# Kernel tuning notes

Hardware: AMD Instinct MI355X
Metric: run time of the kernel (lower is better)

## Reference

```python
import jax, jax.numpy as jnp
import numpy as np

E = 4        # num_edge_types
C = 4        # num_channels (must equal E due to module's layer>0 einsum)
N = 2048     # num_nodes
W_IN = 256
W_OUT = 128


def _xavier_uniform(key, shape):
    # torch.nn.init.xavier_uniform_ on a 2D tensor [fan_out, fan_in] style
    fan_out, fan_in = shape[0], shape[1]
    bound = float(np.sqrt(6.0 / (fan_in + fan_out)))
    return jax.random.uniform(key, shape, jnp.float32, -bound, bound)


def setup_inputs() -> dict:
    key = jax.random.key(0)
    k = jax.random.split(key, 7)
    A = jax.random.uniform(k[0], (E, N, N), jnp.float32)   # non-negative dense multi-relation adjacency
    X = jax.random.normal(k[1], (N, W_IN), jnp.float32)
    gt_w1 = _xavier_uniform(k[2], (C, E))   # layer0 conv1
    gt_w2 = _xavier_uniform(k[3], (C, E))   # layer0 conv2
    gt_w3 = _xavier_uniform(k[4], (C, C))   # layer1 conv1 (C == E)
    gcn_w = _xavier_uniform(k[5], (W_IN, W_OUT))
    gcn_b = jnp.zeros((W_OUT,), jnp.float32)
    return {"A": A, "X": X, "gt_w1": gt_w1, "gt_w2": gt_w2, "gt_w3": gt_w3,
            "gcn_w": gcn_w, "gcn_b": gcn_b}


def _normalize_adj(adj):
    # adj: [N, N]. Symmetric degree normalization D^-1/2 (A+I) D^-1/2,
    # expressed as broadcasted row/col scaling (math-identical to the
    # original diag-matmul-matmul formulation).
    adj = adj + jnp.eye(adj.shape[0], dtype=adj.dtype)
    deg = adj.sum(axis=1)
    d = deg ** -0.5
    d = jnp.where(jnp.isinf(d), jnp.zeros_like(d), d)
    return d[:, None] * adj * d[None, :]


def reference(A, X, gt_w1, gt_w2, gt_w3, gcn_w, gcn_b):
    # --- GT layer 0 (first=True): two softmax-weighted mixes of A, then bmm ---
    fw1 = jax.nn.softmax(gt_w1, axis=1)
    fw2 = jax.nn.softmax(gt_w2, axis=1)
    Ha = jnp.einsum('oi,inm->onm', fw1, A)   # [C, N, N]
    Hb = jnp.einsum('oi,inm->onm', fw2, A)   # [C, N, N]
    H = jnp.matmul(Ha, Hb)                   # [C, N, N]
    # --- GT layer 1 (first=False): H @ (softmax mix of A) ---
    fw3 = jax.nn.softmax(gt_w3, axis=1)
    Hc = jnp.einsum('oi,inm->onm', fw3, A)   # [C, N, N]
    H = jnp.matmul(H, Hc)                    # [C, N, N]
    # --- per-channel degree-normalized GCN conv ---
    Hn = jax.vmap(_normalize_adj)(H)         # [C, N, N]
    support = X @ gcn_w                      # [N, W_OUT] (shared across channels)
    out = jnp.einsum('cnm,mf->cnf', Hn, support) + gcn_b  # [C, N, W_OUT]
    out = jax.nn.relu(out)
    # torch.cat(X_out, dim=1): channel blocks side by side -> [N, C*W_OUT]
    return jnp.transpose(out, (1, 0, 2)).reshape(N, C * W_OUT)
```

## Files before the change

kernel.cpp:

```cpp
#include <hip/hip_runtime.h>
#include <math.h>

#define N_NODES 2048
#define NNE ((long)N_NODES * N_NODES)

#define SUPD_SCALE 8192.0f

typedef _Float16 half4_t __attribute__((ext_vector_type(4)));
typedef _Float16 half8_t __attribute__((ext_vector_type(8)));
typedef float    floatx4 __attribute__((ext_vector_type(4)));

__device__ __forceinline__ void async_cp16(const void* g, void* l) {
  __builtin_amdgcn_global_load_lds((const __attribute__((address_space(1))) void*)g,
                                   (__attribute__((address_space(3))) void*)l,
                                   16, 0, 0);
}

__device__ __forceinline__ float colscale_from(float cn) {
  return exp2f((float)(10 - ilogbf(fmaxf(cn, 1e-37f))));
}

__global__ void softmax3_zero_k(const float* __restrict__ w1,
                                const float* __restrict__ w2,
                                const float* __restrict__ w3,
                                float* __restrict__ fw,
                                float* __restrict__ cn) {
  int t = threadIdx.x;
  float4 z4 = {0.f, 0.f, 0.f, 0.f};
  ((float4*)cn)[t] = z4;
  if (t < 12) {
    const float* src = (t < 4) ? w1 : (t < 8) ? w2 : w3;
    int r = t & 3;
    float v0 = src[r * 4 + 0], v1 = src[r * 4 + 1];
    float v2 = src[r * 4 + 2], v3 = src[r * 4 + 3];
    float m = fmaxf(fmaxf(v0, v1), fmaxf(v2, v3));
    float e0 = expf(v0 - m), e1 = expf(v1 - m), e2 = expf(v2 - m), e3 = expf(v3 - m);
    float inv = 1.0f / (e0 + e1 + e2 + e3);
    fw[t * 4 + 0] = e0 * inv; fw[t * 4 + 1] = e1 * inv;
    fw[t * 4 + 2] = e2 * inv; fw[t * 4 + 3] = e3 * inv;
  }
}

__global__ __launch_bounds__(128)
void support_k(const float* __restrict__ X, const float* __restrict__ W,
               float* __restrict__ sup) {
  __shared__ float Xs[256];
  const int t = threadIdx.x;
  const int m = blockIdx.x;
  Xs[t]       = X[(long)m * 256 + t];
  Xs[t + 128] = X[(long)m * 256 + t + 128];
  __syncthreads();
  float acc = 0.f;
  #pragma unroll 8
  for (int k = 0; k < 256; ++k) acc = fmaf(Xs[k], W[(long)k * 128 + t], acc);
  sup[(long)m * 128 + t] = acc;
}

__global__ __launch_bounds__(256)
void rc_from_A_k(const float* __restrict__ A, const float* __restrict__ fw,
                 float* __restrict__ rc) {
  __shared__ float red[4][4];
  const int r = blockIdx.x;
  const int w = threadIdx.x >> 6, lane = threadIdx.x & 63;
  float se[4];
  #pragma unroll
  for (int e = 0; e < 4; ++e) {
    const float4* row = (const float4*)(A + (long)e * NNE + (long)r * N_NODES);
    float s = 0.f;
    #pragma unroll
    for (int q = 0; q < 2; ++q) {
      float4 a = row[w * 128 + q * 64 + lane];
      s += (a.x + a.y) + (a.z + a.w);
    }
    se[e] = s;
  }
  float m[4];
  #pragma unroll
  for (int c = 0; c < 4; ++c)
    m[c] = fw[32 + c * 4 + 0] * se[0] + fw[32 + c * 4 + 1] * se[1] +
           fw[32 + c * 4 + 2] * se[2] + fw[32 + c * 4 + 3] * se[3];
  #pragma unroll
  for (int o = 32; o > 0; o >>= 1) {
    #pragma unroll
    for (int c = 0; c < 4; ++c) m[c] += __shfl_down(m[c], o, 64);
  }
  if (lane == 0) {
    #pragma unroll
    for (int c = 0; c < 4; ++c) red[w][c] = m[c];
  }
  __syncthreads();
  if (threadIdx.x < 4) {
    int c = threadIdx.x;
    rc[c * N_NODES + r] = (red[0][c] + red[1][c]) + (red[2][c] + red[3][c]);
  }
}

__global__ __launch_bounds__(256)
void matvecA_k(const float* __restrict__ A, const float* __restrict__ fw, int off,
               const float* __restrict__ vin, float* __restrict__ vout) {
  __shared__ float red[4][4];
  const int r = blockIdx.x;
  const int w = threadIdx.x >> 6, lane = threadIdx.x & 63;
  float acc[4][4] = {{0.f}};
  #pragma unroll
  for (int q = 0; q < 2; ++q) {
    const int j4 = w * 128 + q * 64 + lane;
    float4 v0 = *(const float4*)&vin[0 * 2048 + j4 * 4];
    float4 v1 = *(const float4*)&vin[1 * 2048 + j4 * 4];
    float4 v2 = *(const float4*)&vin[2 * 2048 + j4 * 4];
    float4 v3 = *(const float4*)&vin[3 * 2048 + j4 * 4];
    #pragma unroll
    for (int e = 0; e < 4; ++e) {
      float4 a = *(const float4*)(A + (long)e * NNE + (long)r * N_NODES + j4 * 4);
      acc[e][0] += (a.x * v0.x + a.y * v0.y) + (a.z * v0.z + a.w * v0.w);
      acc[e][1] += (a.x * v1.x + a.y * v1.y) + (a.z * v1.z + a.w * v1.w);
      acc[e][2] += (a.x * v2.x + a.y * v2.y) + (a.z * v2.z + a.w * v2.w);
      acc[e][3] += (a.x * v3.x + a.y * v3.y) + (a.z * v3.z + a.w * v3.w);
    }
  }
  float m[4];
  #pragma unroll
  for (int c = 0; c < 4; ++c)
    m[c] = fw[off + c * 4 + 0] * acc[0][c] + fw[off + c * 4 + 1] * acc[1][c] +
           fw[off + c * 4 + 2] * acc[2][c] + fw[off + c * 4 + 3] * acc[3][c];
  #pragma unroll
  for (int o = 32; o > 0; o >>= 1) {
    #pragma unroll
    for (int c = 0; c < 4; ++c) m[c] += __shfl_down(m[c], o, 64);
  }
  if (lane == 0) {
    #pragma unroll
    for (int c = 0; c < 4; ++c) red[w][c] = m[c];
  }
  __syncthreads();
  if (threadIdx.x < 4) {
    int c = threadIdx.x;
    vout[c * N_NODES + r] = (red[0][c] + red[1][c]) + (red[2][c] + red[3][c]);
  }
}

__global__ __launch_bounds__(256)
void transposeV_k(const float* __restrict__ sup, const float* __restrict__ deg,
                  float* __restrict__ dvec, float* __restrict__ supd,
                  _Float16* __restrict__ TH, _Float16* __restrict__ TL,
                  float* __restrict__ cn0) {
  __shared__ _Float16 sh[32][33], sl[32][33];
  __shared__ float red[8][32];
  const int t = threadIdx.x;
  const int z = blockIdx.z;
  const int m0 = blockIdx.x * 32, f0 = blockIdx.y * 32;
  const int r0 = t >> 5, col = t & 31;
  float part = 0.f;
  #pragma unroll
  for (int m = 0; m < 4; ++m) {
    const int row = m0 + r0 + 8 * m;
    float dm = 1.0f / sqrtf(1.0f + deg[(long)z * N_NODES + row]);
    float sv = sup[(long)row * 128 + f0 + col] * dm;
    supd[((long)z * N_NODES + row) * 128 + f0 + col] = sv;
    if (blockIdx.y == 0 && col == 0) dvec[(long)z * N_NODES + row] = dm;
    float v = sv * SUPD_SCALE;
    _Float16 h = (_Float16)v;
    sh[r0 + 8 * m][col] = h;
    sl[r0 + 8 * m][col] = (_Float16)(v - (float)h);
    part += fabsf(v);
  }
  red[r0][col] = part;
  __syncthreads();
  if (t < 32) {
    float s = 0.f;
    #pragma unroll
    for (int q = 0; q < 8; ++q) s += red[q][t];
    atomicAdd(&cn0[(long)z * 128 + f0 + t], s);
  }
  const int rr = t >> 3, cq = (t & 7) * 4;
  half4_t oh, ol;
  #pragma unroll
  for (int d = 0; d < 4; ++d) { oh[d] = sh[cq + d][rr]; ol[d] = sl[cq + d][rr]; }
  long ob = (long)z * 128 * N_NODES + (long)(f0 + rr) * N_NODES + m0 + cq;
  *(half4_t*)(TH + ob) = oh;
  *(half4_t*)(TL + ob) = ol;
}

__global__ __launch_bounds__(256, 4)
void gemm_mix_k(const float* __restrict__ A, const float* __restrict__ fw, int off,
                const _Float16* __restrict__ BH, const _Float16* __restrict__ BL,
                float* __restrict__ C) {
  __shared__ __align__(16) _Float16 Hs[2][2][1024];
  __shared__ __align__(16) _Float16 Bs[2][2][4096];

  const int t = threadIdx.x;
  const int lane = t & 63;
  const int w = t >> 6;
  const int bid = blockIdx.x;
  const int tile = bid & 63;
  const int ch = (bid >> 6) & 3;
  const int kc = bid >> 8;
  const int i0 = tile * 32;
  const long koff = (long)kc * 512;

  float wv[4];
  #pragma unroll
  for (int e = 0; e < 4; ++e) wv[e] = fw[off + ch * 4 + e];

  const int rr = t >> 3;
  const int k4 = (t & 7) * 4;
  const float* gA = A + (long)(i0 + rr) * N_NODES + koff + k4;
  const int hoff = rr * 32 + (((k4 >> 3) + (rr >> 1)) & 3) * 8 + (k4 & 7);

  const int hls = w >> 1;
  const int half = w & 1;
  const int kc_st = (((lane & 3) - ((lane >> 3) & 3)) & 3) * 8;
  const _Float16* gB = (hls ? BL : BH)
                     + ((long)ch * 128 + half * 64 + (lane >> 2)) * (long)N_NODES
                     + koff + kc_st;

  const int wm = w >> 1, wn = w & 1;
  const int fr = lane & 15;
  const int fq = lane >> 4;
  const int fkz = ((fq + (fr >> 1)) & 3) * 8;
  const int aoff = (wm * 16 + fr) * 32 + fkz;

  floatx4 acc[4];
  #pragma unroll
  for (int j = 0; j < 4; ++j) {
    floatx4 zz4 = {0.f, 0.f, 0.f, 0.f};
    acc[j] = zz4;
  }

  const int NKT = 16;

  auto stageB = [&](int ktv, int pb) {
    _Float16* lb = &Bs[pb][hls][half * 2048];
    const _Float16* g = gB + ktv * 32;
    #pragma unroll
    for (int q = 0; q < 4; ++q)
      async_cp16(g + (long)q * (16L * N_NODES), lb + q * 512 + lane * 8);
  };
  auto mixStore = [&](const float4& a0, const float4& a1,
                      const float4& a2, const float4& a3, int pb) {
    float av0[4] = {a0.x, a0.y, a0.z, a0.w};
    float av1[4] = {a1.x, a1.y, a1.z, a1.w};
    float av2[4] = {a2.x, a2.y, a2.z, a2.w};
    float av3[4] = {a3.x, a3.y, a3.z, a3.w};
    half4_t h, l;
    #pragma unroll
    for (int d = 0; d < 4; ++d) {
      float o = wv[0] * av0[d] + wv[1] * av1[d] + wv[2] * av2[d] + wv[3] * av3[d];
      _Float16 hh = (_Float16)o;
      h[d] = hh; l[d] = (_Float16)(o - (float)hh);
    }
    *(half4_t*)&Hs[pb][0][hoff] = h;
    *(half4_t*)&Hs[pb][1][hoff] = l;
  };

  {
    float4 a0 = *(const float4*)(gA);
    float4 a1 = *(const float4*)(gA + NNE);
    float4 a2 = *(const float4*)(gA + 2 * NNE);
    float4 a3 = *(const float4*)(gA + 3 * NNE);
    stageB(0, 0);
    mixStore(a0, a1, a2, a3, 0);
  }
  __syncthreads();

  for (int kt = 0; kt < NKT; ++kt) {
    const int p = kt & 1;
    float4 a0, a1, a2, a3;
    if (kt + 1 < NKT) {
      const float* g = gA + (kt + 1) * 32;
      a0 = *(const float4*)(g);
      a1 = *(const float4*)(g + NNE);
      a2 = *(const float4*)(g + 2 * NNE);
      a3 = *(const float4*)(g + 3 * NNE);
      stageB(kt + 1, p ^ 1);
    }
    half8_t ah = *(const half8_t*)&Hs[p][0][aoff];
    half8_t al = *(const half8_t*)&Hs[p][1][aoff];
    #pragma unroll
    for (int nt = 0; nt < 4; ++nt) {
      const int bo = (wn * 64 + nt * 16 + fr) * 32 + fkz;
      half8_t bh = *(const half8_t*)&Bs[p][0][bo];
      half8_t bl = *(const half8_t*)&Bs[p][1][bo];
      acc[nt] = __builtin_amdgcn_mfma_f32_16x16x32_f16(ah, bh, acc[nt], 0, 0, 0);
      acc[nt] = __builtin_amdgcn_mfma_f32_16x16x32_f16(al, bh, acc[nt], 0, 0, 0);
      acc[nt] = __builtin_amdgcn_mfma_f32_16x16x32_f16(ah, bl, acc[nt], 0, 0, 0);
    }
    if (kt + 1 < NKT) mixStore(a0, a1, a2, a3, p ^ 1);
    __syncthreads();
  }

  const int er = fq * 4;
  const int ec = lane & 15;
  float* Cb = C + ((long)(kc * 4 + ch) * N_NODES + i0 + wm * 16) * 128;
  #pragma unroll
  for (int nt = 0; nt < 4; ++nt) {
    const int f = wn * 64 + nt * 16 + ec;
    #pragma unroll
    for (int r = 0; r < 4; ++r)
      Cb[(long)(er + r) * 128 + f] = acc[nt][r];
  }
}

__global__ __launch_bounds__(256)
void combineT_k(const float* __restrict__ P, int parts,
                const float* __restrict__ cn_in, float* __restrict__ cn_out,
                _Float16* __restrict__ TH, _Float16* __restrict__ TL) {
  __shared__ _Float16 sh[32][33], sl[32][33];
  __shared__ float red[8][32];
  const int t = threadIdx.x;
  const int z = blockIdx.z;
  const int j0 = blockIdx.x * 32, f0 = blockIdx.y * 32;
  const int r0 = t >> 5, col = t & 31;
  const float s = colscale_from(cn_in[(long)z * 128 + f0 + col]);
  const long step = 4L * N_NODES * 128;
  float part = 0.f;
  #pragma unroll
  for (int m = 0; m < 4; ++m) {
    long idx = ((long)z * N_NODES + j0 + r0 + 8 * m) * 128 + f0 + col;
    float v = (P[idx] + P[idx + step]) + (P[idx + 2 * step] + P[idx + 3 * step]);
    v *= s;
    _Float16 h = (_Float16)v;
    sh[r0 + 8 * m][col] = h;
    sl[r0 + 8 * m][col] = (_Float16)(v - (float)h);
    part += fabsf(v);
  }
  if (cn_out) red[r0][col] = part;
  __syncthreads();
  if (cn_out && t < 32) {
    float ss = 0.f;
    #pragma unroll
    for (int q = 0; q < 8; ++q) ss += red[q][t];
    atomicAdd(&cn_out[(long)z * 128 + f0 + t], ss);
  }
  const int rr = t >> 3, cq = (t & 7) * 4;
  half4_t oh, ol;
  #pragma unroll
  for (int d = 0; d < 4; ++d) { oh[d] = sh[cq + d][rr]; ol[d] = sl[cq + d][rr]; }
  long ob = (long)z * 128 * N_NODES + (long)(f0 + rr) * N_NODES + j0 + cq;
  *(half4_t*)(TH + ob) = oh;
  *(half4_t*)(TL + ob) = ol;
}

__global__ __launch_bounds__(256)
void final_k(const float4* __restrict__ T2, const float4* __restrict__ supd,
             const float* __restrict__ dvec, const float* __restrict__ cn0,
             const float* __restrict__ cn1, const float* __restrict__ bias,
             float* __restrict__ out) {
  const int t = threadIdx.x;
  const int z = blockIdx.y;
  const int idx = blockIdx.x * 256 + t;
  const int i = idx >> 5;
  const int fq = (idx & 31) * 4;
  const long step4 = 4L * N_NODES * 32;
  long b4 = (long)z * N_NODES * 32 + idx;
  float4 s0 = T2[b4];
  float4 s1 = T2[b4 + step4];
  float4 s2 = T2[b4 + 2 * step4];
  float4 s3 = T2[b4 + 3 * step4];
  float4 sp = supd[(long)z * N_NODES * 32 + idx];
  const float dn = dvec[(long)z * N_NODES + i];
  float inv[4];
  #pragma unroll
  for (int d = 0; d < 4; ++d) {
    int i0 = ilogbf(fmaxf(cn0[(long)z * 128 + fq + d], 1e-37f));
    int i1 = ilogbf(fmaxf(cn1[(long)z * 128 + fq + d], 1e-37f));
    inv[d] = exp2f((float)(i0 + i1 - 33));
  }
  float4 o;
  o.x = fmaxf(dn * (((s0.x + s1.x) + (s2.x + s3.x)) * inv[0] + sp.x) + bias[fq + 0], 0.f);
  o.y = fmaxf(dn * (((s0.y + s1.y) + (s2.y + s3.y)) * inv[1] + sp.y) + bias[fq + 1], 0.f);
  o.z = fmaxf(dn * (((s0.z + s1.z) + (s2.z + s3.z)) * inv[2] + sp.z) + bias[fq + 2], 0.f);
  o.w = fmaxf(dn * (((s0.w + s1.w) + (s2.w + s3.w)) * inv[3] + sp.w) + bias[fq + 3], 0.f);
  *(float4*)(out + (long)i * 512 + z * 128 + fq) = o;
}

extern "C" void kernel_launch(void* const* d_in, const int* in_sizes, int n_in,
                              void* d_out, int out_size, void* d_ws, size_t ws_size,
                              hipStream_t stream) {
  const float* A  = (const float*)d_in[0];
  const float* X  = (const float*)d_in[1];
  const float* w1 = (const float*)d_in[2];
  const float* w2 = (const float*)d_in[3];
  const float* w3 = (const float*)d_in[4];
  const float* gw = (const float*)d_in[5];
  const float* gb = (const float*)d_in[6];
  float* out = (float*)d_out;

  float* ws   = (float*)d_ws;
  float* fw   = ws;
  float* rc   = fw + 64;
  float* v1   = rc + 4 * N_NODES;
  float* deg  = v1 + 4 * N_NODES;
  float* dvec = deg + 4 * N_NODES;
  float* sup  = dvec + 4 * N_NODES;
  float* cn0  = sup + (long)N_NODES * 128;
  float* cn1  = cn0 + 512;
  float* supd = cn1 + 512;
  float* Mtmp = supd + 4L * N_NODES * 128;
  _Float16* arena = (_Float16*)(Mtmp + 16L * N_NODES * 128);
  _Float16* VTH = arena;
  _Float16* VTL = VTH + 4L * 128 * N_NODES;
  _Float16* T0H = VTL + 4L * 128 * N_NODES;
  _Float16* T0L = T0H + 4L * 128 * N_NODES;
  _Float16* T1H = T0L + 4L * 128 * N_NODES;
  _Float16* T1L = T1H + 4L * 128 * N_NODES;

  softmax3_zero_k<<<1, 256, 0, stream>>>(w1, w2, w3, fw, cn0);
  support_k<<<N_NODES, 128, 0, stream>>>(X, gw, sup);
  rc_from_A_k<<<N_NODES, 256, 0, stream>>>(A, fw, rc);
  matvecA_k<<<N_NODES, 256, 0, stream>>>(A, fw, 16, rc, v1);
  matvecA_k<<<N_NODES, 256, 0, stream>>>(A, fw, 0, v1, deg);
  transposeV_k<<<dim3(64, 4, 4), 256, 0, stream>>>(sup, deg, dvec, supd,
                                                   VTH, VTL, cn0);
  gemm_mix_k<<<1024, 256, 0, stream>>>(A, fw, 32, VTH, VTL, Mtmp);
  combineT_k<<<dim3(64, 4, 4), 256, 0, stream>>>(Mtmp, 4, cn0, cn1, T0H, T0L);
  gemm_mix_k<<<1024, 256, 0, stream>>>(A, fw, 16, T0H, T0L, Mtmp);
  combineT_k<<<dim3(64, 4, 4), 256, 0, stream>>>(Mtmp, 4, cn1, nullptr, T1H, T1L);
  gemm_mix_k<<<1024, 256, 0, stream>>>(A, fw, 0, T1H, T1L, Mtmp);
  final_k<<<dim3(256, 4), 256, 0, stream>>>((const float4*)Mtmp,
                                            (const float4*)supd, dvec,
                                            cn0, cn1, gb, out);
}
```

Baseline: 259.7 us.

## Load GEMM B operands directly into registers and drop the supd buffer

The GEMM kernel stops staging the B tiles (high/low fp16 halves) through LDS with async global-to-LDS copies. Each wave now loads its MFMA B fragments straight from global memory into registers, double-buffered across two k-steps, and the LDS B buffer and the occupancy hint in the launch bounds are removed. Separately, the intermediate supd buffer is no longer written; final_k rebuilds that term from sup scaled by dn squared. The aims are lower LDS traffic and footprint and one fewer global write and read, at the cost of more VGPRs and less coalesced, possibly redundant global loads of B across waves.

```diff
diff --git a/kernel.cpp b/kernel.cpp
--- a/kernel.cpp
+++ b/kernel.cpp
@@ -9,12 +9,6 @@
 typedef _Float16 half4_t __attribute__((ext_vector_type(4)));
 typedef _Float16 half8_t __attribute__((ext_vector_type(8)));
 typedef float    floatx4 __attribute__((ext_vector_type(4)));
-
-__device__ __forceinline__ void async_cp16(const void* g, void* l) {
-  __builtin_amdgcn_global_load_lds((const __attribute__((address_space(1))) void*)g,
-                                   (__attribute__((address_space(3))) void*)l,
-                                   16, 0, 0);
-}
 
 __device__ __forceinline__ float colscale_from(float cn) {
   return exp2f((float)(10 - ilogbf(fmaxf(cn, 1e-37f))));
@@ -141,7 +135,7 @@
 
 __global__ __launch_bounds__(256)
 void transposeV_k(const float* __restrict__ sup, const float* __restrict__ deg,
-                  float* __restrict__ dvec, float* __restrict__ supd,
+                  float* __restrict__ dvec,
                   _Float16* __restrict__ TH, _Float16* __restrict__ TL,
                   float* __restrict__ cn0) {
   __shared__ _Float16 sh[32][33], sl[32][33];
@@ -156,7 +150,6 @@
     const int row = m0 + r0 + 8 * m;
     float dm = 1.0f / sqrtf(1.0f + deg[(long)z * N_NODES + row]);
     float sv = sup[(long)row * 128 + f0 + col] * dm;
-    supd[((long)z * N_NODES + row) * 128 + f0 + col] = sv;
     if (blockIdx.y == 0 && col == 0) dvec[(long)z * N_NODES + row] = dm;
     float v = sv * SUPD_SCALE;
     _Float16 h = (_Float16)v;
@@ -181,12 +174,11 @@
   *(half4_t*)(TL + ob) = ol;
 }
 
-__global__ __launch_bounds__(256, 4)
+__global__ __launch_bounds__(256)
 void gemm_mix_k(const float* __restrict__ A, const float* __restrict__ fw, int off,
                 const _Float16* __restrict__ BH, const _Float16* __restrict__ BL,
                 float* __restrict__ C) {
   __shared__ __align__(16) _Float16 Hs[2][2][1024];
-  __shared__ __align__(16) _Float16 Bs[2][2][4096];
 
   const int t = threadIdx.x;
   const int lane = t & 63;
@@ -207,19 +199,16 @@
   const float* gA = A + (long)(i0 + rr) * N_NODES + koff + k4;
   const int hoff = rr * 32 + (((k4 >> 3) + (rr >> 1)) & 3) * 8 + (k4 & 7);
 
-  const int hls = w >> 1;
-  const int half = w & 1;
-  const int kc_st = (((lane & 3) - ((lane >> 3) & 3)) & 3) * 8;
-  const _Float16* gB = (hls ? BL : BH)
-                     + ((long)ch * 128 + half * 64 + (lane >> 2)) * (long)N_NODES
-                     + koff + kc_st;
-
   const int wm = w >> 1, wn = w & 1;
   const int fr = lane & 15;
   const int fq = lane >> 4;
   const int fkz = ((fq + (fr >> 1)) & 3) * 8;
   const int aoff = (wm * 16 + fr) * 32 + fkz;
 
+  const long bbase = ((long)(ch * 128 + wn * 64 + fr)) * N_NODES + koff + fq * 8;
+  const _Float16* gBH = BH + bbase;
+  const _Float16* gBL = BL + bbase;
+
   floatx4 acc[4];
   #pragma unroll
   for (int j = 0; j < 4; ++j) {
@@ -227,65 +216,64 @@
     acc[j] = zz4;
   }
 
-  const int NKT = 16;
-
-  auto stageB = [&](int ktv, int pb) {
-    _Float16* lb = &Bs[pb][hls][half * 2048];
-    const _Float16* g = gB + ktv * 32;
-    #pragma unroll
-    for (int q = 0; q < 4; ++q)
-      async_cp16(g + (long)q * (16L * N_NODES), lb + q * 512 + lane * 8);
+  float4 aA[4], aB[4];
+  half8_t b0h[4], b0l[4], b1h[4], b1l[4];
+
+  auto loadA = [&](float4* av, int kt) {
+    const float* g = gA + kt * 32;
+    av[0] = *(const float4*)(g);
+    av[1] = *(const float4*)(g + NNE);
+    av[2] = *(const float4*)(g + 2 * NNE);
+    av[3] = *(const float4*)(g + 3 * NNE);
   };
-  auto mixStore = [&](const float4& a0, const float4& a1,
-                      const float4& a2, const float4& a3, int pb) {
-    float av0[4] = {a0.x, a0.y, a0.z, a0.w};
-    float av1[4] = {a1.x, a1.y, a1.z, a1.w};
-    float av2[4] = {a2.x, a2.y, a2.z, a2.w};
-    float av3[4] = {a3.x, a3.y, a3.z, a3.w};
+  auto loadB = [&](half8_t* bh, half8_t* bl, int kt) {
+    #pragma unroll
+    for (int nt = 0; nt < 4; ++nt) {
+      bh[nt] = *(const half8_t*)(gBH + (long)nt * 16 * N_NODES + kt * 32);
+      bl[nt] = *(const half8_t*)(gBL + (long)nt * 16 * N_NODES + kt * 32);
+    }
+  };
+  auto mixStore = [&](const float4* av, int pb) {
     half4_t h, l;
     #pragma unroll
     for (int d = 0; d < 4; ++d) {
-      float o = wv[0] * av0[d] + wv[1] * av1[d] + wv[2] * av2[d] + wv[3] * av3[d];
+      float o = wv[0] * ((const float*)&av[0])[d] + wv[1] * ((const float*)&av[1])[d] +
+                wv[2] * ((const float*)&av[2])[d] + wv[3] * ((const float*)&av[3])[d];
       _Float16 hh = (_Float16)o;
       h[d] = hh; l[d] = (_Float16)(o - (float)hh);
     }
     *(half4_t*)&Hs[pb][0][hoff] = h;
     *(half4_t*)&Hs[pb][1][hoff] = l;
   };
-
-  {
-    float4 a0 = *(const float4*)(gA);
-    float4 a1 = *(const float4*)(gA + NNE);
-    float4 a2 = *(const float4*)(gA + 2 * NNE);
-    float4 a3 = *(const float4*)(gA + 3 * NNE);
-    stageB(0, 0);
-    mixStore(a0, a1, a2, a3, 0);
-  }
-  __syncthreads();
-
-  for (int kt = 0; kt < NKT; ++kt) {
-    const int p = kt & 1;
-    float4 a0, a1, a2, a3;
-    if (kt + 1 < NKT) {
-      const float* g = gA + (kt + 1) * 32;
-      a0 = *(const float4*)(g);
-      a1 = *(const float4*)(g + NNE);
-      a2 = *(const float4*)(g + 2 * NNE);
-      a3 = *(const float4*)(g + 3 * NNE);
-      stageB(kt + 1, p ^ 1);
-    }
-    half8_t ah = *(const half8_t*)&Hs[p][0][aoff];
-    half8_t al = *(const half8_t*)&Hs[p][1][aoff];
+  auto domfma = [&](int pb, const half8_t* bh, const half8_t* bl) {
+    half8_t ah = *(const half8_t*)&Hs[pb][0][aoff];
+    half8_t al = *(const half8_t*)&Hs[pb][1][aoff];
     #pragma unroll
     for (int nt = 0; nt < 4; ++nt) {
-      const int bo = (wn * 64 + nt * 16 + fr) * 32 + fkz;
-      half8_t bh = *(const half8_t*)&Bs[p][0][bo];
-      half8_t bl = *(const half8_t*)&Bs[p][1][bo];
-      acc[nt] = __builtin_amdgcn_mfma_f32_16x16x32_f16(ah, bh, acc[nt], 0, 0, 0);
-      acc[nt] = __builtin_amdgcn_mfma_f32_16x16x32_f16(al, bh, acc[nt], 0, 0, 0);
-      acc[nt] = __builtin_amdgcn_mfma_f32_16x16x32_f16(ah, bl, acc[nt], 0, 0, 0);
-    }
-    if (kt + 1 < NKT) mixStore(a0, a1, a2, a3, p ^ 1);
+      acc[nt] = __builtin_amdgcn_mfma_f32_16x16x32_f16(ah, bh[nt], acc[nt], 0, 0, 0);
+      acc[nt] = __builtin_amdgcn_mfma_f32_16x16x32_f16(al, bh[nt], acc[nt], 0, 0, 0);
+      acc[nt] = __builtin_amdgcn_mfma_f32_16x16x32_f16(ah, bl[nt], acc[nt], 0, 0, 0);
+    }
+  };
+
+  loadA(aA, 0); loadB(b0h, b0l, 0);
+  mixStore(aA, 0);
+  loadA(aB, 1); loadB(b1h, b1l, 1);
+  __syncthreads();
+
+  for (int kt = 0; kt < 16; kt += 2) {
+    const bool more = (kt + 2 < 16);
+    if (more) loadA(aA, kt + 2);
+    domfma(0, b0h, b0l);
+    if (more) loadB(b0h, b0l, kt + 2);
+    mixStore(aB, 1);
+    __syncthreads();
+    if (more) loadA(aB, kt + 3);
+    domfma(1, b1h, b1l);
+    if (more) {
+      loadB(b1h, b1l, kt + 3);
+      mixStore(aA, 0);
+    }
     __syncthreads();
   }
 
@@ -342,7 +330,7 @@
 }
 
 __global__ __launch_bounds__(256)
-void final_k(const float4* __restrict__ T2, const float4* __restrict__ supd,
+void final_k(const float4* __restrict__ T2, const float4* __restrict__ sup4,
              const float* __restrict__ dvec, const float* __restrict__ cn0,
              const float* __restrict__ cn1, const float* __restrict__ bias,
              float* __restrict__ out) {
@@ -357,20 +345,21 @@
   float4 s1 = T2[b4 + step4];
   float4 s2 = T2[b4 + 2 * step4];
   float4 s3 = T2[b4 + 3 * step4];
-  float4 sp = supd[(long)z * N_NODES * 32 + idx];
+  float4 su = sup4[idx];
   const float dn = dvec[(long)z * N_NODES + i];
+  const float dn2 = dn * dn;
   float inv[4];
   #pragma unroll
   for (int d = 0; d < 4; ++d) {
     int i0 = ilogbf(fmaxf(cn0[(long)z * 128 + fq + d], 1e-37f));
     int i1 = ilogbf(fmaxf(cn1[(long)z * 128 + fq + d], 1e-37f));
-    inv[d] = exp2f((float)(i0 + i1 - 33));
+    inv[d] = exp2f((float)(i0 + i1 - 33)) * dn;
   }
   float4 o;
-  o.x = fmaxf(dn * (((s0.x + s1.x) + (s2.x + s3.x)) * inv[0] + sp.x) + bias[fq + 0], 0.f);
-  o.y = fmaxf(dn * (((s0.y + s1.y) + (s2.y + s3.y)) * inv[1] + sp.y) + bias[fq + 1], 0.f);
-  o.z = fmaxf(dn * (((s0.z + s1.z) + (s2.z + s3.z)) * inv[2] + sp.z) + bias[fq + 2], 0.f);
-  o.w = fmaxf(dn * (((s0.w + s1.w) + (s2.w + s3.w)) * inv[3] + sp.w) + bias[fq + 3], 0.f);
+  o.x = fmaxf(((s0.x + s1.x) + (s2.x + s3.x)) * inv[0] + dn2 * su.x + bias[fq + 0], 0.f);
+  o.y = fmaxf(((s0.y + s1.y) + (s2.y + s3.y)) * inv[1] + dn2 * su.y + bias[fq + 1], 0.f);
+  o.z = fmaxf(((s0.z + s1.z) + (s2.z + s3.z)) * inv[2] + dn2 * su.z + bias[fq + 2], 0.f);
+  o.w = fmaxf(((s0.w + s1.w) + (s2.w + s3.w)) * inv[3] + dn2 * su.w + bias[fq + 3], 0.f);
   *(float4*)(out + (long)i * 512 + z * 128 + fq) = o;
 }
 
@@ -395,8 +384,7 @@
   float* sup  = dvec + 4 * N_NODES;
   float* cn0  = sup + (long)N_NODES * 128;
   float* cn1  = cn0 + 512;
-  float* supd = cn1 + 512;
-  float* Mtmp = supd + 4L * N_NODES * 128;
+  float* Mtmp = cn1 + 512;
   _Float16* arena = (_Float16*)(Mtmp + 16L * N_NODES * 128);
   _Float16* VTH = arena;
   _Float16* VTL = VTH + 4L * 128 * N_NODES;
@@ -410,7 +398,7 @@
   rc_from_A_k<<<N_NODES, 256, 0, stream>>>(A, fw, rc);
   matvecA_k<<<N_NODES, 256, 0, stream>>>(A, fw, 16, rc, v1);
   matvecA_k<<<N_NODES, 256, 0, stream>>>(A, fw, 0, v1, deg);
-  transposeV_k<<<dim3(64, 4, 4), 256, 0, stream>>>(sup, deg, dvec, supd,
+  transposeV_k<<<dim3(64, 4, 4), 256, 0, stream>>>(sup, deg, dvec,
                                                    VTH, VTL, cn0);
   gemm_mix_k<<<1024, 256, 0, stream>>>(A, fw, 32, VTH, VTL, Mtmp);
   combineT_k<<<dim3(64, 4, 4), 256, 0, stream>>>(Mtmp, 4, cn0, cn1, T0H, T0L);
@@ -418,6 +406,6 @@
   combineT_k<<<dim3(64, 4, 4), 256, 0, stream>>>(Mtmp, 4, cn1, nullptr, T1H, T1L);
   gemm_mix_k<<<1024, 256, 0, stream>>>(A, fw, 0, T1H, T1L, Mtmp);
   final_k<<<dim3(256, 4), 256, 0, stream>>>((const float4*)Mtmp,
-                                            (const float4*)supd, dvec,
+                                            (const float4*)sup, dvec,
                                             cn0, cn1, gb, out);
 }
```

New measurement: 363.4 us. 1.4x slower.
